# Performance work log

Measured on AMD Instinct MI355X. Metric: run time of the kernel, lower is better.

The kernel has to match this reference:

```python
import jax, jax.numpy as jnp
import numpy as np

N = 50000   # nodes
E = 800000  # edges (avg degree 16)
D = 128     # in_dim = out_dim
H = 8       # heads
O = D // H  # per-head dim = 16
FF = 512    # ffn inner hidden
LN_EPS = 1e-6
LRELU_SLOPE = 0.01  # torch F.leaky_relu default


def setup_inputs() -> dict:
    key = jax.random.key(0)
    ks = jax.random.split(key, 9)
    x = jax.random.normal(ks[0], (N, D), jnp.float32)
    src = jax.random.randint(ks[1], (E,), 0, N)
    dst = jax.random.randint(ks[2], (E,), 0, N)
    fc_w = jax.random.normal(ks[3], (H, D, O), jnp.float32) * 0.05
    a_l = jax.random.normal(ks[4], (H, O), jnp.float32) * 0.05
    a_r = jax.random.normal(ks[5], (H, O), jnp.float32) * 0.05
    w1 = jax.random.normal(ks[6], (D, FF), jnp.float32) * 0.05
    b1 = jnp.zeros((FF,), jnp.float32)
    w2 = jax.random.normal(ks[7], (FF, D), jnp.float32) * 0.05
    b2 = jnp.zeros((D,), jnp.float32)
    ln_g = jnp.ones((D,), jnp.float32)
    ln_b = jnp.zeros((D,), jnp.float32)
    return dict(x=x, fc_w=fc_w, a_l=a_l, a_r=a_r, ln_g=ln_g, ln_b=ln_b,
                w1=w1, b1=b1, w2=w2, b2=b2, src=src, dst=dst)


def _gat_s2s(x, fc_w, a_l, a_r, src, dst):
    # per-head projection: [N,H,O]
    z = jnp.einsum('nd,hdo->nho', x, fc_w)
    # attn_fc([z_src||z_dst]) == a_l . z_src + a_r . z_dst  (decomposed, same math)
    el = jnp.einsum('nho,ho->nh', z, a_l)  # [N,H]
    er = jnp.einsum('nho,ho->nh', z, a_r)  # [N,H]
    e = jax.nn.leaky_relu(el[src] + er[dst], LRELU_SLOPE)  # [E,H]
    # edge softmax over incoming edges of each dst node (numerically stable)
    m = jax.ops.segment_max(e, dst, num_segments=N)  # [N,H]
    m = jnp.where(jnp.isfinite(m), m, 0.0)
    ex = jnp.exp(e - m[dst])  # [E,H]
    denom = jax.ops.segment_sum(ex, dst, num_segments=N)  # [N,H]
    alpha = ex / denom[dst]  # [E,H]
    # weighted aggregation of source features: [N,H,O]
    agg = jax.ops.segment_sum(alpha[:, :, None] * z[src], dst, num_segments=N)
    return agg.reshape(N, H * O)  # head concat -> [N,D]


def _ffn(h, ln_g, ln_b, w1, b1, w2, b2):
    # pre-LayerNorm positionwise FFN with gelu and residual (dropout off / eval)
    mu = jnp.mean(h, axis=-1, keepdims=True)
    var = jnp.mean((h - mu) ** 2, axis=-1, keepdims=True)
    ln = (h - mu) * jax.lax.rsqrt(var + LN_EPS) * ln_g + ln_b
    inter = jax.nn.gelu(ln @ w1 + b1, approximate=False)
    return inter @ w2 + b2 + h


def reference(x, fc_w, a_l, a_r, ln_g, ln_b, w1, b1, w2, b2, src, dst):
    h = jax.nn.elu(_gat_s2s(x, fc_w, a_l, a_r, src, dst))
    h = h + x  # residual with origin (S2S: origin == neighbor == x)
    return _ffn(h, ln_g, ln_b, w1, b1, w2, b2)
```

## Files before the change

kernel.cpp:

```cpp
#include <hip/hip_runtime.h>

#define NN 50000
#define EE 800000
#define LDK 136
#define SLOTS 64
#define FEPT 8

#define C_X    0
#define C_ZW   6400000
#define C_AL   6416384
#define C_AR   6416512
#define C_LNG  6416640
#define C_LNB  6416768
#define C_W1T  6416896
#define C_B1   6482432
#define C_W2T  6482944
#define C_B2   6548480
#define C_WAT  6548608
#define C_TOT  6550656

typedef __attribute__((ext_vector_type(8))) short bf16x8;
typedef __attribute__((ext_vector_type(4))) float f32x4;

__device__ __forceinline__ float bf2f(unsigned short u) {
  union { unsigned int i; float f; } v; v.i = ((unsigned int)u) << 16; return v.f;
}
__device__ __forceinline__ unsigned short f2bf(float f) {
  union { float f; unsigned int i; } v; v.f = f;
  unsigned int r = v.i + 0x7fffu + ((v.i >> 16) & 1u);
  return (unsigned short)(r >> 16);
}
__device__ __forceinline__ int ld_idx(const void* p, int i, int is64) {
  return is64 ? (int)((const long long*)p)[i] : ((const int*)p)[i];
}

__device__ __forceinline__ float fast_gelu(float u) {
  float ax = fabsf(u) * 0.70710678118654752f;
  float d  = fmaf(0.3275911f, ax, 1.f);
  float r  = __builtin_amdgcn_rcpf(d);
  r = r * fmaf(-d, r, 2.f);
  float p = fmaf(1.061405429f, r, -1.453152027f);
  p = fmaf(p, r, 1.421413741f);
  p = fmaf(p, r, -0.284496736f);
  p = fmaf(p, r, 0.254829592f);
  p = p * r;
  float e = __expf(-ax * ax);
  float erfv = fmaf(-p, e, 1.f);
  union { float f; unsigned int i; } su, se;
  su.f = u; se.f = erfv;
  se.i = se.i | (su.i & 0x80000000u);
  return 0.5f * u * (1.f + se.f);
}

__global__ void k_probe(const unsigned short* __restrict__ xr,
                        const int* __restrict__ s, const int* __restrict__ d,
                        int* __restrict__ flags) {
  int i = blockIdx.x * 256 + threadIdx.x;
  int bad = 0, zc = 0, zs = 0, zd = 0;
  for (int j = i; j < 65536; j += 32 * 256) {
    unsigned short u = xr[j];
    if ((u & 0x7F80u) == 0x7F80u) bad = 1;
    if (((j & 1) == 0) && u == 0) zc++;
  }
  for (int j = i; j < 131072; j += 32 * 256) {
    if (j & 1) {
      if (s[j] == 0) zs++;
      if (d[j] == 0) zd++;
    }
  }
  if (bad) atomicOr(&flags[0], 1);
  if (zc) atomicAdd(&flags[1], zc);
  if (zs) atomicAdd(&flags[2], zs);
  if (zd) atomicAdd(&flags[3], zd);
}

__global__ __launch_bounds__(256) void k_convert(
    const void* __restrict__ x, const void* __restrict__ fcw,
    const void* __restrict__ a_l, const void* __restrict__ a_r,
    const void* __restrict__ lng, const void* __restrict__ lnb,
    const void* __restrict__ w1, const void* __restrict__ b1,
    const void* __restrict__ w2, const void* __restrict__ b2,
    const int* __restrict__ flag, unsigned short* __restrict__ canon) {
  const int isf32 = (flag[0] != 0) || (flag[1] > 8192);
  const int tid0 = blockIdx.x * 256 + threadIdx.x;
  for (int v = tid0; v < (C_ZW >> 3); v += gridDim.x * 256) {
    if (isf32) {
      const float* xf = (const float*)x + v * 8;
      float4 a = *(const float4*)xf;
      float4 b = *(const float4*)(xf + 4);
      union { unsigned short u[8]; uint4 q; } pk;
      pk.u[0] = f2bf(a.x); pk.u[1] = f2bf(a.y); pk.u[2] = f2bf(a.z); pk.u[3] = f2bf(a.w);
      pk.u[4] = f2bf(b.x); pk.u[5] = f2bf(b.y); pk.u[6] = f2bf(b.z); pk.u[7] = f2bf(b.w);
      *(uint4*)(canon + v * 8) = pk.q;
    } else {
      *(uint4*)(canon + v * 8) = *(const uint4*)((const unsigned short*)x + v * 8);
    }
  }
  for (int i = C_ZW + tid0; i < C_TOT; i += gridDim.x * 256) {
    unsigned short v;
    if (i >= C_WAT) {
      int j = i - C_WAT; int c = j >> 7, dd = j & 127; int h = c & 7;
      const void* fa = (c < 8) ? a_l : a_r;
      float s = 0.f;
      if (isf32) {
        const float* fw = (const float*)fcw + h * 2048 + dd * 16;
        const float* fv = (const float*)fa + h * 16;
#pragma unroll
        for (int o = 0; o < 16; o++) s += fw[o] * fv[o];
      } else {
        const unsigned short* fw = (const unsigned short*)fcw + h * 2048 + dd * 16;
        const unsigned short* fv = (const unsigned short*)fa + h * 16;
#pragma unroll
        for (int o = 0; o < 16; o++) s += bf2f(fw[o]) * bf2f(fv[o]);
      }
      v = f2bf(s);
    } else {
      const void* src; int idx;
      if (i < C_AL)       { int j = i - C_ZW; int c = j >> 7, d = j & 127; src = fcw; idx = (c >> 4) * 2048 + d * 16 + (c & 15); }
      else if (i < C_AR)  { src = a_l; idx = i - C_AL; }
      else if (i < C_LNG) { src = a_r; idx = i - C_AR; }
      else if (i < C_LNB) { src = lng; idx = i - C_LNG; }
      else if (i < C_W1T) { src = lnb; idx = i - C_LNB; }
      else if (i < C_B1)  { int j = i - C_W1T; int n = j >> 7, k = j & 127; src = w1; idx = k * 512 + n; }
      else if (i < C_W2T) { src = b1;  idx = i - C_B1; }
      else if (i < C_B2)  { int j = i - C_W2T; int n = j >> 9, k = j & 511; src = w2; idx = k * 128 + n; }
      else                { src = b2;  idx = i - C_B2; }
      if (isf32) v = f2bf(((const float*)src)[idx]);
      else       v = ((const unsigned short*)src)[idx];
    }
    canon[i] = v;
  }
}

__global__ __launch_bounds__(256) void k_project(
    const unsigned short* __restrict__ canon,
    unsigned short* __restrict__ z, float* __restrict__ el, float* __restrict__ er) {
  const unsigned short* xc  = canon + C_X;
  const unsigned short* zwt = canon + C_ZW;
  const unsigned short* wat = canon + C_WAT;
  __shared__ unsigned short sA[128 * LDK];
  __shared__ unsigned short sB[64 * LDK];
  const int tid = threadIdx.x;
  const int row0 = (blockIdx.x >> 1) * 128;
  const int n0 = (blockIdx.x & 1) * 64;
  for (int v = tid; v < 2048; v += 256) {
    int r = v >> 4, k8 = (v & 15) << 3;
    int gr = row0 + r; if (gr >= NN) gr = NN - 1;
    *(uint4*)(&sA[r * LDK + k8]) = *(const uint4*)(xc + gr * 128 + k8);
  }
  for (int v = tid; v < 1024; v += 256) {
    int n = v >> 4, k8 = (v & 15) << 3;
    *(uint4*)(&sB[n * LDK + k8]) = *(const uint4*)(zwt + (n0 + n) * 128 + k8);
  }
  __syncthreads();
  const int lane = tid & 63, w = tid >> 6;
  const int mr = lane & 15, q = lane >> 4;
  const f32x4 zero = {0.f, 0.f, 0.f, 0.f};
  f32x4 acc[8];
#pragma unroll
  for (int i = 0; i < 8; i++) acc[i] = zero;
#pragma unroll
  for (int kc = 0; kc < 4; kc++) {
    bf16x8 b = *(const bf16x8*)(&sB[(w * 16 + mr) * LDK + kc * 32 + q * 8]);
#pragma unroll
    for (int mt = 0; mt < 8; mt++) {
      bf16x8 a = *(const bf16x8*)(&sA[(mt * 16 + mr) * LDK + kc * 32 + q * 8]);
      acc[mt] = __builtin_amdgcn_mfma_f32_16x16x32_bf16(a, b, acc[mt], 0, 0, 0);
    }
  }
  const int col = n0 + w * 16 + mr;
#pragma unroll
  for (int mt = 0; mt < 8; mt++) {
#pragma unroll
    for (int r = 0; r < 4; r++) {
      int grow = row0 + mt * 16 + q * 4 + r;
      if (grow < NN) z[grow * 128 + col] = f2bf(acc[mt][r]);
    }
  }
  if (n0 == 0) {
    f32x4 e0 = zero, e1 = zero;
#pragma unroll
    for (int kc = 0; kc < 4; kc++) {
      bf16x8 b = *(const bf16x8*)(wat + mr * 128 + kc * 32 + q * 8);
      bf16x8 a0 = *(const bf16x8*)(&sA[(w * 16 + mr) * LDK + kc * 32 + q * 8]);
      bf16x8 a1 = *(const bf16x8*)(&sA[((w + 4) * 16 + mr) * LDK + kc * 32 + q * 8]);
      e0 = __builtin_amdgcn_mfma_f32_16x16x32_bf16(a0, b, e0, 0, 0, 0);
      e1 = __builtin_amdgcn_mfma_f32_16x16x32_bf16(a1, b, e1, 0, 0, 0);
    }
    float* eo = (mr < 8) ? el : er;
    const int hh = mr & 7;
#pragma unroll
    for (int r = 0; r < 4; r++) {
      int g0 = row0 + w * 16 + q * 4 + r;
      int g1 = row0 + (w + 4) * 16 + q * 4 + r;
      if (g0 < NN) eo[g0 * 8 + hh] = e0[r];
      if (g1 < NN) eo[g1 * 8 + hh] = e1[r];
    }
  }
}

__global__ __launch_bounds__(256) void k_fill(const void* __restrict__ src,
                                              const void* __restrict__ dst,
                                              const int* __restrict__ iflags,
                                              int* __restrict__ cnt,
                                              unsigned short* __restrict__ esrc) {
  const int base = (blockIdx.x * 256 + threadIdx.x) * FEPT;
  if (base >= EE) return;
  const int s64 = iflags[0] > 1000, d64 = iflags[1] > 1000;
  int dv[FEPT], sv[FEPT];
  if (!d64 && base + FEPT <= EE) {
    const int4* p = (const int4*)((const int*)dst + base);
    int4 a = p[0], b = p[1];
    dv[0]=a.x; dv[1]=a.y; dv[2]=a.z; dv[3]=a.w; dv[4]=b.x; dv[5]=b.y; dv[6]=b.z; dv[7]=b.w;
  } else {
#pragma unroll
    for (int j = 0; j < FEPT; j++) dv[j] = (base + j < EE) ? ld_idx(dst, base + j, d64) : 0;
  }
  if (!s64 && base + FEPT <= EE) {
    const int4* p = (const int4*)((const int*)src + base);
    int4 a = p[0], b = p[1];
    sv[0]=a.x; sv[1]=a.y; sv[2]=a.z; sv[3]=a.w; sv[4]=b.x; sv[5]=b.y; sv[6]=b.z; sv[7]=b.w;
  } else {
#pragma unroll
    for (int j = 0; j < FEPT; j++) sv[j] = (base + j < EE) ? ld_idx(src, base + j, s64) : 0;
  }
#pragma unroll
  for (int j = 0; j < FEPT; j++) {
    if (base + j < EE) {
      unsigned d = (unsigned)dv[j]; if (d >= NN) d = 0;
      unsigned s = (unsigned)sv[j]; if (s >= NN) s = 0;
      int p = atomicAdd(&cnt[d], 1);
      if (p < SLOTS) esrc[d * SLOTS + p] = (unsigned short)s;
    }
  }
}

__global__ __launch_bounds__(256) void k_agg(
    const unsigned short* __restrict__ canon, const unsigned short* __restrict__ z,
    const float* __restrict__ el, const float* __restrict__ er,
    const int* __restrict__ cnt, const unsigned short* __restrict__ esrc,
    const void* __restrict__ srcp, const void* __restrict__ dstp,
    const int* __restrict__ iflags,
    float* __restrict__ h1out, float2* __restrict__ mars) {
  const unsigned short* xc = canon + C_X;
  const int lane = threadIdx.x & 63;
  const int node = blockIdx.x * 4 + (threadIdx.x >> 6);
  if (node >= NN) return;
  const int degr = cnt[node];
  const int hl = lane & 7;
  const int g  = lane >> 3;
  const float ern = er[node * 8 + hl];

  float m = -3.0e38f;
  float acc[16];
#pragma unroll
  for (int j = 0; j < 16; j++) acc[j] = 0.f;
  float denom = 0.f;

  if (degr <= SLOTS) {
    const int deg = degr;
    const unsigned short* eptr = esrc + node * SLOTS;
    for (int b = 0; b < deg; b += 16) {
      int e0 = b + g, e1 = b + g + 8;
      int c0 = (e0 < deg) ? e0 : deg - 1;
      int c1 = (e1 < deg) ? e1 : deg - 1;
      unsigned s0 = eptr[c0]; if (s0 >= NN) s0 = 0;
      unsigned s1 = eptr[c1]; if (s1 >= NN) s1 = 0;
      float t0 = el[s0 * 8 + hl] + ern;
      float t1 = el[s1 * 8 + hl] + ern;
      t0 = (t0 > 0.f) ? t0 : 0.01f * t0;
      t1 = (t1 > 0.f) ? t1 : 0.01f * t1;
      if (e0 < deg) m = fmaxf(m, t0);
      if (e1 < deg) m = fmaxf(m, t1);
    }
    m = fmaxf(m, __shfl_xor(m, 8));
    m = fmaxf(m, __shfl_xor(m, 16));
    m = fmaxf(m, __shfl_xor(m, 32));
    for (int b = 0; b < deg; b += 16) {
      int e0 = b + g, e1 = b + g + 8;
      int c0 = (e0 < deg) ? e0 : deg - 1;
      int c1 = (e1 < deg) ? e1 : deg - 1;
      unsigned s0 = eptr[c0]; if (s0 >= NN) s0 = 0;
      unsigned s1 = eptr[c1]; if (s1 >= NN) s1 = 0;
      float t0 = el[s0 * 8 + hl] + ern;
      float t1 = el[s1 * 8 + hl] + ern;
      bf16x8 za0 = *(const bf16x8*)(z + s0 * 128 + hl * 16);
      bf16x8 za1 = *(const bf16x8*)(z + s0 * 128 + hl * 16 + 8);
      bf16x8 zb0 = *(const bf16x8*)(z + s1 * 128 + hl * 16);
      bf16x8 zb1 = *(const bf16x8*)(z + s1 * 128 + hl * 16 + 8);
      t0 = (t0 > 0.f) ? t0 : 0.01f * t0;
      t1 = (t1 > 0.f) ? t1 : 0.01f * t1;
      float ex0 = (e0 < deg) ? __expf(fminf(t0 - m, 0.f)) : 0.f;
      float ex1 = (e1 < deg) ? __expf(fminf(t1 - m, 0.f)) : 0.f;
      denom += ex0 + ex1;
#pragma unroll
      for (int j = 0; j < 8; j++) {
        acc[j]     += ex0 * bf2f((unsigned short)za0[j]) + ex1 * bf2f((unsigned short)zb0[j]);
        acc[j + 8] += ex0 * bf2f((unsigned short)za1[j]) + ex1 * bf2f((unsigned short)zb1[j]);
      }
    }
  } else {
    const int s64 = iflags[0] > 1000, d64 = iflags[1] > 1000;
    for (int b = 0; b < EE; b += 8) {
      int e = b + g;
      unsigned dd = (unsigned)ld_idx(dstp, e, d64); if (dd >= NN) dd = 0;
      bool ok = (dd == (unsigned)node);
      unsigned s0 = (unsigned)ld_idx(srcp, e, s64); if (s0 >= NN) s0 = 0;
      float t0 = el[s0 * 8 + hl] + ern;
      t0 = (t0 > 0.f) ? t0 : 0.01f * t0;
      if (ok) m = fmaxf(m, t0);
    }
    m = fmaxf(m, __shfl_xor(m, 8));
    m = fmaxf(m, __shfl_xor(m, 16));
    m = fmaxf(m, __shfl_xor(m, 32));
    for (int b = 0; b < EE; b += 8) {
      int e = b + g;
      unsigned dd = (unsigned)ld_idx(dstp, e, d64); if (dd >= NN) dd = 0;
      bool ok = (dd == (unsigned)node);
      unsigned s0 = (unsigned)ld_idx(srcp, e, s64); if (s0 >= NN) s0 = 0;
      float t0 = el[s0 * 8 + hl] + ern;
      t0 = (t0 > 0.f) ? t0 : 0.01f * t0;
      float ex0 = ok ? __expf(fminf(t0 - m, 0.f)) : 0.f;
      denom += ex0;
      bf16x8 za0 = *(const bf16x8*)(z + s0 * 128 + hl * 16);
      bf16x8 za1 = *(const bf16x8*)(z + s0 * 128 + hl * 16 + 8);
#pragma unroll
      for (int j = 0; j < 8; j++) {
        acc[j]     += ex0 * bf2f((unsigned short)za0[j]);
        acc[j + 8] += ex0 * bf2f((unsigned short)za1[j]);
      }
    }
  }

  denom += __shfl_xor(denom, 8);
  denom += __shfl_xor(denom, 16);
  denom += __shfl_xor(denom, 32);
  {
    const bool hi1 = (lane & 32) != 0;
#pragma unroll
    for (int j = 0; j < 8; j++) {
      float send = hi1 ? acc[j] : acc[j + 8];
      float recv = __shfl_xor(send, 32);
      float keep = hi1 ? acc[j + 8] : acc[j];
      acc[j] = keep + recv;
    }
    const bool hi2 = (lane & 16) != 0;
#pragma unroll
    for (int j = 0; j < 4; j++) {
      float send = hi2 ? acc[j] : acc[j + 4];
      float recv = __shfl_xor(send, 16);
      float keep = hi2 ? acc[j + 4] : acc[j];
      acc[j] = keep + recv;
    }
    const bool hi3 = (lane & 8) != 0;
#pragma unroll
    for (int j = 0; j < 2; j++) {
      float send = hi3 ? acc[j] : acc[j + 2];
      float recv = __shfl_xor(send, 8);
      float keep = hi3 ? acc[j + 2] : acc[j];
      acc[j] = keep + recv;
    }
  }
  const float inv = (denom > 0.f) ? 1.f / denom : 0.f;
  const int c = hl * 16 + g * 2;
  float r0 = acc[0] * inv;
  float r1 = acc[1] * inv;
  unsigned int xx = *(const unsigned int*)(xc + node * 128 + c);
  float hv0 = ((r0 > 0.f) ? r0 : (__expf(fminf(r0, 0.f)) - 1.f)) + bf2f((unsigned short)(xx & 0xffffu));
  float hv1 = ((r1 > 0.f) ? r1 : (__expf(fminf(r1, 0.f)) - 1.f)) + bf2f((unsigned short)(xx >> 16));
  float s1 = hv0 + hv1;
  float s2 = hv0 * hv0 + hv1 * hv1;
#pragma unroll
  for (int off = 1; off < 64; off <<= 1) {
    s1 += __shfl_xor(s1, off);
    s2 += __shfl_xor(s2, off);
  }
  if (lane == 0) {
    float mu = s1 * (1.f / 128.f);
    float var = s2 * (1.f / 128.f) - mu * mu;
    mars[node] = make_float2(mu, rsqrtf(fmaxf(var, 0.f) + 1e-6f));
  }
  *(float2*)(h1out + node * 128 + c) = make_float2(hv0, hv1);
}

__global__ __launch_bounds__(512) void k_ffn(
    const unsigned short* __restrict__ canon, const float2* __restrict__ mars,
    float* __restrict__ out) {
  const unsigned short* lngc = canon + C_LNG;
  const unsigned short* lnbc = canon + C_LNB;
  const unsigned short* w1t  = canon + C_W1T;
  const unsigned short* b1c  = canon + C_B1;
  const unsigned short* w2t  = canon + C_W2T;
  const unsigned short* b2c  = canon + C_B2;
  __shared__ unsigned short sLn[64 * LDK];
  __shared__ unsigned short sInt[64 * LDK];
  const int tid = threadIdx.x;
  const int row0 = blockIdx.x * 64;
  {
    const int r = tid >> 3, t8 = tid & 7;
    const int grow = row0 + r;
    const int gr = (grow < NN) ? grow : NN - 1;
    const float2 ms = mars[gr];
    const float* hrow = out + (size_t)gr * 128 + t8 * 16;
#pragma unroll
    for (int h8 = 0; h8 < 2; h8++) {
      float4 a = *(const float4*)(hrow + h8 * 8);
      float4 b = *(const float4*)(hrow + h8 * 8 + 4);
      union { unsigned short u[8]; uint4 q; } gv, bv, pk;
      gv.q = *(const uint4*)(lngc + t8 * 16 + h8 * 8);
      bv.q = *(const uint4*)(lnbc + t8 * 16 + h8 * 8);
      float vv[8] = {a.x, a.y, a.z, a.w, b.x, b.y, b.z, b.w};
#pragma unroll
      for (int j = 0; j < 8; j++)
        pk.u[j] = f2bf((vv[j] - ms.x) * ms.y * bf2f(gv.u[j]) + bf2f(bv.u[j]));
      *(uint4*)(&sLn[r * LDK + t8 * 16 + h8 * 8]) = pk.q;
    }
  }
  __syncthreads();
  const int lane = tid & 63, w = tid >> 6;
  const int mr = lane & 15, q = lane >> 4;
  const f32x4 zero = {0.f, 0.f, 0.f, 0.f};
  f32x4 acc2[4];
#pragma unroll
  for (int a = 0; a < 4; a++) acc2[a] = zero;
#pragma unroll
  for (int qr = 0; qr < 4; qr++) {
    if (qr) __syncthreads();
    const int colg = qr * 128 + w * 16;
    f32x4 a1[4];
#pragma unroll
    for (int a = 0; a < 4; a++) a1[a] = zero;
#pragma unroll
    for (int kc = 0; kc < 4; kc++) {
      bf16x8 wf = *(const bf16x8*)(w1t + (colg + mr) * 128 + kc * 32 + q * 8);
#pragma unroll
      for (int rt = 0; rt < 4; rt++) {
        bf16x8 lf = *(const bf16x8*)(&sLn[(rt * 16 + mr) * LDK + kc * 32 + q * 8]);
        a1[rt] = __builtin_amdgcn_mfma_f32_16x16x32_bf16(wf, lf, a1[rt], 0, 0, 0);
      }
    }
    union { unsigned short u[4]; uint2 v; } b1v;
    b1v.v = *(const uint2*)(b1c + colg + q * 4);
#pragma unroll
    for (int rt = 0; rt < 4; rt++) {
      union { unsigned short u[4]; uint2 v; } pk;
#pragma unroll
      for (int r = 0; r < 4; r++)
        pk.u[r] = f2bf(fast_gelu(a1[rt][r] + bf2f(b1v.u[r])));
      *(uint2*)(&sInt[(rt * 16 + mr) * LDK + w * 16 + q * 4]) = pk.v;
    }
    __syncthreads();
#pragma unroll
    for (int ks = 0; ks < 4; ks++) {
      bf16x8 bw = *(const bf16x8*)(w2t + (w * 16 + mr) * 512 + qr * 128 + ks * 32 + q * 8);
#pragma unroll
      for (int mt = 0; mt < 4; mt++) {
        bf16x8 af = *(const bf16x8*)(&sInt[(mt * 16 + mr) * LDK + ks * 32 + q * 8]);
        acc2[mt] = __builtin_amdgcn_mfma_f32_16x16x32_bf16(af, bw, acc2[mt], 0, 0, 0);
      }
    }
  }
  {
    const int col = w * 16 + mr;
    const float bias = bf2f(b2c[col]);
#pragma unroll
    for (int mt = 0; mt < 4; mt++)
#pragma unroll
      for (int r = 0; r < 4; r++) {
        int grow = row0 + mt * 16 + q * 4 + r;
        if (grow < NN) {
          size_t o = (size_t)grow * 128 + col;
          out[o] = acc2[mt][r] + bias + out[o];
        }
      }
  }
}

extern "C" void kernel_launch(void* const* d_in, const int* in_sizes, int n_in,
                              void* d_out, int out_size, void* d_ws, size_t ws_size,
                              hipStream_t stream) {
  const void* x   = d_in[0];
  const void* fcw = d_in[1];
  const void* a_l = d_in[2];
  const void* a_r = d_in[3];
  const void* lng = d_in[4];
  const void* lnb = d_in[5];
  const void* w1  = d_in[6];
  const void* b1  = d_in[7];
  const void* w2  = d_in[8];
  const void* b2  = d_in[9];
  const void* src = d_in[10];
  const void* dst = d_in[11];
  float* out = (float*)d_out;

  char* ws = (char*)d_ws;
  size_t off = 0;
  auto alloc = [&](size_t bytes) -> char* {
    char* p = ws + off; off += (bytes + 255) & ~(size_t)255; return p;
  };
  int* flags            = (int*)alloc(64);
  int* fflags           = flags;
  int* iflags           = flags + 2;
  int* cnt              = (int*)alloc((size_t)NN * 4);
  unsigned short* esrc  = (unsigned short*)alloc((size_t)NN * SLOTS * 2);
  unsigned short* canon = (unsigned short*)alloc((size_t)C_TOT * 2);
  unsigned short* z     = (unsigned short*)alloc((size_t)NN * 128 * 2);
  float* el             = (float*)alloc((size_t)NN * 8 * 4);
  float* er             = (float*)alloc((size_t)NN * 8 * 4);
  float2* mars          = (float2*)alloc((size_t)NN * 8);

  hipMemsetAsync(ws, 0, 256 + (size_t)NN * 4, stream);
  k_probe<<<32, 256, 0, stream>>>((const unsigned short*)x, (const int*)src, (const int*)dst, flags);
  k_convert<<<2048, 256, 0, stream>>>(x, fcw, a_l, a_r, lng, lnb, w1, b1, w2, b2, fflags, canon);
  k_project<<<391 * 2, 256, 0, stream>>>(canon, z, el, er);
  k_fill<<<(EE + 256 * FEPT - 1) / (256 * FEPT), 256, 0, stream>>>(src, dst, iflags, cnt, esrc);
  k_agg<<<(NN + 3) / 4, 256, 0, stream>>>(canon, z, el, er, cnt, esrc, src, dst, iflags, out, mars);
  k_ffn<<<(NN + 63) / 64, 512, 0, stream>>>(canon, mars, out);
}
```

Before: 263.5 us.

## Fuse edge-bucket fill into convert and projection kernels as extra blocks

```diff
diff --git a/kernel.cpp b/kernel.cpp
--- a/kernel.cpp
+++ b/kernel.cpp
@@ -5,6 +5,10 @@
 #define LDK 136
 #define SLOTS 64
 #define FEPT 8
+#define NFA 157
+#define SPLITE (NFA * 256 * FEPT)
+#define NFB 234
+#define CONVB 2048
 
 #define C_X    0
 #define C_ZW   6400000
@@ -74,16 +78,58 @@
   if (zd) atomicAdd(&flags[3], zd);
 }
 
-__global__ __launch_bounds__(256) void k_convert(
+__device__ __forceinline__ void do_fill(const void* __restrict__ src,
+                                        const void* __restrict__ dst,
+                                        const int* __restrict__ iflags,
+                                        int* __restrict__ cnt,
+                                        unsigned short* __restrict__ esrc,
+                                        int base) {
+  if (base >= EE) return;
+  const int s64 = iflags[0] > 1000, d64 = iflags[1] > 1000;
+  int dv[FEPT], sv[FEPT];
+  if (!d64 && base + FEPT <= EE) {
+    const int4* p = (const int4*)((const int*)dst + base);
+    int4 a = p[0], b = p[1];
+    dv[0]=a.x; dv[1]=a.y; dv[2]=a.z; dv[3]=a.w; dv[4]=b.x; dv[5]=b.y; dv[6]=b.z; dv[7]=b.w;
+  } else {
+#pragma unroll
+    for (int j = 0; j < FEPT; j++) dv[j] = (base + j < EE) ? ld_idx(dst, base + j, d64) : 0;
+  }
+  if (!s64 && base + FEPT <= EE) {
+    const int4* p = (const int4*)((const int*)src + base);
+    int4 a = p[0], b = p[1];
+    sv[0]=a.x; sv[1]=a.y; sv[2]=a.z; sv[3]=a.w; sv[4]=b.x; sv[5]=b.y; sv[6]=b.z; sv[7]=b.w;
+  } else {
+#pragma unroll
+    for (int j = 0; j < FEPT; j++) sv[j] = (base + j < EE) ? ld_idx(src, base + j, s64) : 0;
+  }
+#pragma unroll
+  for (int j = 0; j < FEPT; j++) {
+    if (base + j < EE) {
+      unsigned d = (unsigned)dv[j]; if (d >= NN) d = 0;
+      unsigned s = (unsigned)sv[j]; if (s >= NN) s = 0;
+      int p = atomicAdd(&cnt[d], 1);
+      if (p < SLOTS) esrc[d * SLOTS + p] = (unsigned short)s;
+    }
+  }
+}
+
+__global__ __launch_bounds__(256) void k_convfill(
     const void* __restrict__ x, const void* __restrict__ fcw,
     const void* __restrict__ a_l, const void* __restrict__ a_r,
     const void* __restrict__ lng, const void* __restrict__ lnb,
     const void* __restrict__ w1, const void* __restrict__ b1,
     const void* __restrict__ w2, const void* __restrict__ b2,
-    const int* __restrict__ flag, unsigned short* __restrict__ canon) {
-  const int isf32 = (flag[0] != 0) || (flag[1] > 8192);
-  const int tid0 = blockIdx.x * 256 + threadIdx.x;
-  for (int v = tid0; v < (C_ZW >> 3); v += gridDim.x * 256) {
+    const int* __restrict__ flags, unsigned short* __restrict__ canon,
+    const void* __restrict__ srcp, const void* __restrict__ dstp,
+    int* __restrict__ cnt, unsigned short* __restrict__ esrc) {
+  if (blockIdx.x < NFA) {
+    do_fill(srcp, dstp, flags + 2, cnt, esrc, (blockIdx.x * 256 + threadIdx.x) * FEPT);
+    return;
+  }
+  const int isf32 = (flags[0] != 0) || (flags[1] > 8192);
+  const int tid0 = (blockIdx.x - NFA) * 256 + threadIdx.x;
+  for (int v = tid0; v < (C_ZW >> 3); v += CONVB * 256) {
     if (isf32) {
       const float* xf = (const float*)x + v * 8;
       float4 a = *(const float4*)xf;
@@ -96,7 +142,7 @@
       *(uint4*)(canon + v * 8) = *(const uint4*)((const unsigned short*)x + v * 8);
     }
   }
-  for (int i = C_ZW + tid0; i < C_TOT; i += gridDim.x * 256) {
+  for (int i = C_ZW + tid0; i < C_TOT; i += CONVB * 256) {
     unsigned short v;
     if (i >= C_WAT) {
       int j = i - C_WAT; int c = j >> 7, dd = j & 127; int h = c & 7;
@@ -132,17 +178,26 @@
   }
 }
 
-__global__ __launch_bounds__(256) void k_project(
+__global__ __launch_bounds__(256) void k_projfill(
     const unsigned short* __restrict__ canon,
-    unsigned short* __restrict__ z, float* __restrict__ el, float* __restrict__ er) {
+    unsigned short* __restrict__ z, float* __restrict__ el, float* __restrict__ er,
+    const void* __restrict__ srcp, const void* __restrict__ dstp,
+    const int* __restrict__ iflags,
+    int* __restrict__ cnt, unsigned short* __restrict__ esrc) {
+  __shared__ unsigned short sA[128 * LDK];
+  __shared__ unsigned short sB[64 * LDK];
+  if (blockIdx.x < NFB) {
+    do_fill(srcp, dstp, iflags, cnt, esrc,
+            SPLITE + (blockIdx.x * 256 + threadIdx.x) * FEPT);
+    return;
+  }
+  const int pid = blockIdx.x - NFB;
   const unsigned short* xc  = canon + C_X;
   const unsigned short* zwt = canon + C_ZW;
   const unsigned short* wat = canon + C_WAT;
-  __shared__ unsigned short sA[128 * LDK];
-  __shared__ unsigned short sB[64 * LDK];
   const int tid = threadIdx.x;
-  const int row0 = (blockIdx.x >> 1) * 128;
-  const int n0 = (blockIdx.x & 1) * 64;
+  const int row0 = (pid >> 1) * 128;
+  const int n0 = (pid & 1) * 64;
   for (int v = tid; v < 2048; v += 256) {
     int r = v >> 4, k8 = (v & 15) << 3;
     int gr = row0 + r; if (gr >= NN) gr = NN - 1;
@@ -195,42 +250,6 @@
       int g1 = row0 + (w + 4) * 16 + q * 4 + r;
       if (g0 < NN) eo[g0 * 8 + hh] = e0[r];
       if (g1 < NN) eo[g1 * 8 + hh] = e1[r];
-    }
-  }
-}
-
-__global__ __launch_bounds__(256) void k_fill(const void* __restrict__ src,
-                                              const void* __restrict__ dst,
-                                              const int* __restrict__ iflags,
-                                              int* __restrict__ cnt,
-                                              unsigned short* __restrict__ esrc) {
-  const int base = (blockIdx.x * 256 + threadIdx.x) * FEPT;
-  if (base >= EE) return;
-  const int s64 = iflags[0] > 1000, d64 = iflags[1] > 1000;
-  int dv[FEPT], sv[FEPT];
-  if (!d64 && base + FEPT <= EE) {
-    const int4* p = (const int4*)((const int*)dst + base);
-    int4 a = p[0], b = p[1];
-    dv[0]=a.x; dv[1]=a.y; dv[2]=a.z; dv[3]=a.w; dv[4]=b.x; dv[5]=b.y; dv[6]=b.z; dv[7]=b.w;
-  } else {
-#pragma unroll
-    for (int j = 0; j < FEPT; j++) dv[j] = (base + j < EE) ? ld_idx(dst, base + j, d64) : 0;
-  }
-  if (!s64 && base + FEPT <= EE) {
-    const int4* p = (const int4*)((const int*)src + base);
-    int4 a = p[0], b = p[1];
-    sv[0]=a.x; sv[1]=a.y; sv[2]=a.z; sv[3]=a.w; sv[4]=b.x; sv[5]=b.y; sv[6]=b.z; sv[7]=b.w;
-  } else {
-#pragma unroll
-    for (int j = 0; j < FEPT; j++) sv[j] = (base + j < EE) ? ld_idx(src, base + j, s64) : 0;
-  }
-#pragma unroll
-  for (int j = 0; j < FEPT; j++) {
-    if (base + j < EE) {
-      unsigned d = (unsigned)dv[j]; if (d >= NN) d = 0;
-      unsigned s = (unsigned)sv[j]; if (s >= NN) s = 0;
-      int p = atomicAdd(&cnt[d], 1);
-      if (p < SLOTS) esrc[d * SLOTS + p] = (unsigned short)s;
     }
   }
 }
@@ -499,7 +518,6 @@
     char* p = ws + off; off += (bytes + 255) & ~(size_t)255; return p;
   };
   int* flags            = (int*)alloc(64);
-  int* fflags           = flags;
   int* iflags           = flags + 2;
   int* cnt              = (int*)alloc((size_t)NN * 4);
   unsigned short* esrc  = (unsigned short*)alloc((size_t)NN * SLOTS * 2);
@@ -511,9 +529,9 @@
 
   hipMemsetAsync(ws, 0, 256 + (size_t)NN * 4, stream);
   k_probe<<<32, 256, 0, stream>>>((const unsigned short*)x, (const int*)src, (const int*)dst, flags);
-  k_convert<<<2048, 256, 0, stream>>>(x, fcw, a_l, a_r, lng, lnb, w1, b1, w2, b2, fflags, canon);
-  k_project<<<391 * 2, 256, 0, stream>>>(canon, z, el, er);
-  k_fill<<<(EE + 256 * FEPT - 1) / (256 * FEPT), 256, 0, stream>>>(src, dst, iflags, cnt, esrc);
+  k_convfill<<<NFA + CONVB, 256, 0, stream>>>(x, fcw, a_l, a_r, lng, lnb, w1, b1, w2, b2,
+                                              flags, canon, src, dst, cnt, esrc);
+  k_projfill<<<NFB + 391 * 2, 256, 0, stream>>>(canon, z, el, er, src, dst, iflags, cnt, esrc);
   k_agg<<<(NN + 3) / 4, 256, 0, stream>>>(canon, z, el, er, cnt, esrc, src, dst, iflags, out, mars);
   k_ffn<<<(NN + 63) / 64, 512, 0, stream>>>(canon, mars, out);
 }
```

Result: faster. 242.2 us, median of 2 (-8.1%).
